# Kernel tuning notes

Hardware: AMD Instinct MI355X
Metric: run time of the kernel (lower is better)

The kernel has to match this reference:

```python
import jax, jax.numpy as jnp
import numpy as np

N = 100000   # nodes
E = 1250000  # directed edges
F = 32       # node_features
H = 64       # hidden_channels
C = 10       # num_classes
NEG_SLOPE = 0.2  # GATConv default LeakyReLU slope


def _glorot(key, shape):
    fan_in = shape[0]
    return jax.random.normal(key, shape, jnp.float32) / np.sqrt(fan_in)


def setup_inputs() -> dict:
    k = jax.random.split(jax.random.key(0), 16)
    x = jax.random.normal(k[0], (N, F), jnp.float32)
    edge_index = jax.random.randint(k[1], (2, E), 0, N, dtype=jnp.int32)
    return {
        "x": x,
        "edge_index": edge_index,
        # GCNConv 1
        "W1": _glorot(k[2], (F, H)), "b1": jnp.zeros((H,), jnp.float32),
        # GATConv (heads=1)
        "W2": _glorot(k[3], (H, H)),
        "a_src": _glorot(k[4], (H,)), "a_dst": _glorot(k[5], (H,)),
        "b2": jnp.zeros((H,), jnp.float32),
        # GCNConv 3
        "W3": _glorot(k[6], (H, H)), "b3": jnp.zeros((H,), jnp.float32),
        # optimization head
        "Wopt": _glorot(k[7], (H, C)), "bopt": jnp.zeros((C,), jnp.float32),
        # bottleneck detector MLP
        "Wb1": _glorot(k[8], (H, 32)), "bb1": jnp.zeros((32,), jnp.float32),
        "Wb2": _glorot(k[9], (32, 1)), "bb2": jnp.zeros((1,), jnp.float32),
    }


def _gcn_conv(x, W, b, src, dst, n):
    # PyG GCNConv: self-loops already appended to src/dst by caller.
    h = x @ W  # [n, out]
    deg = jnp.zeros((n,), x.dtype).at[dst].add(1.0)
    dinv = jax.lax.rsqrt(jnp.maximum(deg, 1e-12))
    norm = dinv[src] * dinv[dst]  # [e]
    msg = h[src] * norm[:, None]  # gather + scale
    out = jnp.zeros_like(h).at[dst].add(msg)  # scatter-add
    return out + b


def _gat_conv(x, W, a_src, a_dst, b, src, dst, n):
    # PyG GATConv, heads=1: self-loops already appended.
    h = x @ W  # [n, out]
    alpha_s = h @ a_src  # [n]
    alpha_d = h @ a_dst  # [n]
    e = jax.nn.leaky_relu(alpha_s[src] + alpha_d[dst], NEG_SLOPE)  # [e]
    # softmax over incoming edges of each dst node
    emax = jax.ops.segment_max(e, dst, num_segments=n)
    p = jnp.exp(e - emax[dst])
    denom = jax.ops.segment_sum(p, dst, num_segments=n)
    alpha = p / denom[dst]
    out = jnp.zeros_like(h).at[dst].add(h[src] * alpha[:, None])
    return out + b


def reference(x, edge_index, W1, b1, W2, a_src, a_dst, b2, W3, b3,
              Wopt, bopt, Wb1, bb1, Wb2, bb2):
    n = x.shape[0]
    loops = jnp.arange(n, dtype=edge_index.dtype)
    src = jnp.concatenate([edge_index[0], loops])
    dst = jnp.concatenate([edge_index[1], loops])

    h = jax.nn.relu(_gcn_conv(x, W1, b1, src, dst, n))
    h = jax.nn.relu(_gat_conv(h, W2, a_src, a_dst, b2, src, dst, n))
    h = jax.nn.relu(_gcn_conv(h, W3, b3, src, dst, n))

    optimizations = h @ Wopt + bopt                     # [n, C]
    bottlenecks = jax.nn.sigmoid(jax.nn.relu(h @ Wb1 + bb1) @ Wb2 + bb2)  # [n, 1]
    graph_embedding = h.mean(axis=0)                    # [H]
    return optimizations, bottlenecks, graph_embedding
```

## Files before the change

### kernel.cpp

```cpp
#include <hip/hip_runtime.h>
#include <hip/hip_bf16.h>


#define CAP 64
#define NP2 128
#define NB2MAX 800

__device__ __forceinline__ int uwave(){
  return __builtin_amdgcn_readfirstlane(threadIdx.x >> 6);
}
__device__ __forceinline__ unsigned short f2bf(float f){
  unsigned u = __float_as_uint(f);
  return (unsigned short)((u + 0x7fffu + ((u >> 16) & 1u)) >> 16);
}
__device__ __forceinline__ float bfl(unsigned u){ return __uint_as_float(u << 16); }
__device__ __forceinline__ float bfh(unsigned u){ return __uint_as_float(u & 0xffff0000u); }
__device__ __forceinline__ float bfu(unsigned short s){ return __uint_as_float(((unsigned)s) << 16); }
__device__ __forceinline__ float rdlane(float v, int l){
  return __uint_as_float(__builtin_amdgcn_readlane(__float_as_uint(v), l));
}

__global__ void k_setup(const float* __restrict__ Wopt, const float* __restrict__ bopt,
                        const float* __restrict__ Wb1, const float* __restrict__ bb1,
                        float* __restrict__ Wcat, float* __restrict__ bcat,
                        int* __restrict__ bcnt, unsigned short* __restrict__ tb,
                        unsigned short* __restrict__ xh, float* __restrict__ emb_acc,
                        float* __restrict__ als, int n, int nb2){
  int i = blockIdx.x*blockDim.x + threadIdx.x;
  if (i < nb2) bcnt[i] = 0;
  if (blockIdx.x == 0){
    int tid = threadIdx.x;
    for (int j = tid; j < 4096; j += 256){
      int f = j >> 6, c = j & 63;
      float w = 0.f;
      if (c < 10)       w = Wopt[f*10 + c];
      else if (c >= 32) w = Wb1[f*32 + (c-32)];
      Wcat[j] = w;
    }
    if (tid < 64){
      float b = 0.f;
      if (tid < 10)       b = bopt[tid];
      else if (tid >= 32) b = bb1[tid-32];
      bcat[tid] = b;
      tb[(size_t)n*64 + tid] = 0;
      emb_acc[tid] = 0.f;
      if (tid == 0) als[n] = 0.f;
    }
    if (tid >= 64 && tid < 96) xh[(size_t)n*32 + (tid-64)] = 0;
  }
}

__global__ __launch_bounds__(256) void k_part(const int* __restrict__ src,
                        const int* __restrict__ dst,
                        uint2* __restrict__ pairs, int* __restrict__ bcnt,
                        int e, int nb2, int pbcap){
  __shared__ int lcnt[NB2MAX];
  __shared__ int lbase[NB2MAX];
  int tid = threadIdx.x;
  for (int j = tid; j < nb2; j += 256) lcnt[j] = 0;
  __syncthreads();
  int i0 = blockIdx.x*2048 + tid*8;
  int d[8], s[8], bk[8], lp[8];
  int nv = e - i0;
  if (nv > 8) nv = 8;
  if (nv < 0) nv = 0;
  if (nv == 8){
    int4 d0 = *(const int4*)(dst + i0), d1 = *(const int4*)(dst + i0 + 4);
    int4 s0 = *(const int4*)(src + i0), s1 = *(const int4*)(src + i0 + 4);
    d[0]=d0.x; d[1]=d0.y; d[2]=d0.z; d[3]=d0.w;
    d[4]=d1.x; d[5]=d1.y; d[6]=d1.z; d[7]=d1.w;
    s[0]=s0.x; s[1]=s0.y; s[2]=s0.z; s[3]=s0.w;
    s[4]=s1.x; s[5]=s1.y; s[6]=s1.z; s[7]=s1.w;
  } else {
    #pragma unroll
    for (int j = 0; j < 8; j++){ d[j] = 0; s[j] = 0; }
    for (int j = 0; j < nv; j++){ d[j] = dst[i0+j]; s[j] = src[i0+j]; }
  }
  #pragma unroll
  for (int j = 0; j < 8; j++){
    if (j < nv){
      bk[j] = d[j] >> 7;
      lp[j] = atomicAdd(&lcnt[bk[j]], 1);
    }
  }
  __syncthreads();
  for (int j = tid; j < nb2; j += 256){
    int c = lcnt[j];
    if (c) lbase[j] = atomicAdd(&bcnt[j], c);
  }
  __syncthreads();
  #pragma unroll
  for (int j = 0; j < 8; j++){
    if (j < nv){
      int p = lbase[bk[j]] + lp[j];
      if (p < pbcap)
        pairs[(size_t)bk[j]*pbcap + p] = make_uint2((unsigned)d[j], (unsigned)s[j]);
    }
  }
}

__global__ __launch_bounds__(256) void k_fill(const uint2* __restrict__ pairs,
                        const int* __restrict__ bcnt, int* __restrict__ cnt,
                        int* __restrict__ adj, int pbcap, int n){
  __shared__ int lc[NP2];
  __shared__ int ladj[NP2*CAP];
  int b = blockIdx.x;
  int lo = b << 7;
  int nn = min(NP2, n - lo);
  int tid = threadIdx.x;
  for (int j = tid; j < NP2; j += 256) lc[j] = 0;
  int4 nfill = make_int4(n, n, n, n);
  for (int j = tid; j < NP2*CAP/4; j += 256) ((int4*)ladj)[j] = nfill;
  __syncthreads();
  int m = bcnt[b];
  if (m > pbcap) m = pbcap;
  const uint2* pb = pairs + (size_t)b*pbcap;
  for (int j = tid; j < m; j += 256){
    uint2 p = pb[j];
    int r = (int)p.x - lo;
    int pos = atomicAdd(&lc[r], 1);
    if (pos < CAP) ladj[(r << 6) + pos] = (int)p.y;
  }
  __syncthreads();
  if (tid < nn) cnt[lo + tid] = lc[tid];
  int tot = nn << 4;
  uint4* ga = (uint4*)(adj + (size_t)lo*CAP);
  const uint4* la = (const uint4*)ladj;
  for (int j = tid; j < tot; j += 256) ga[j] = la[j];
}

__global__ void k_castscale(const float* __restrict__ x, const int* __restrict__ cnt,
                            unsigned short* __restrict__ xh, int total4){
  int i = blockIdx.x*blockDim.x + threadIdx.x;
  if (i >= total4) return;
  int row = i >> 3;
  float dv = rsqrtf((float)(cnt[row] + 1));
  float4 v = ((const float4*)x)[i];
  uint2 o;
  o.x = (unsigned)f2bf(v.x*dv) | ((unsigned)f2bf(v.y*dv) << 16);
  o.y = (unsigned)f2bf(v.z*dv) | ((unsigned)f2bf(v.w*dv) << 16);
  ((uint2*)xh)[i] = o;
}

__global__ __launch_bounds__(256) void k_agg32g(const unsigned short* __restrict__ xh,
                          const int* __restrict__ adj, const int* __restrict__ cnt,
                          const float* __restrict__ W1, const float* __restrict__ b1,
                          unsigned short* __restrict__ h, int n){
  int lane = threadIdx.x & 63;
  float wreg[32];
  #pragma unroll
  for (int k = 0; k < 32; k++) wreg[k] = W1[k*64 + lane];
  float br = b1[lane];
  int v0 = blockIdx.x*8 + uwave()*2;
  if (v0 >= n) return;
  int v1 = v0 + 1;
  bool has1 = v1 < n;
  if (!has1) v1 = v0;
  int cn0 = cnt[v0], cn1 = cnt[v1];
  int c0 = min(cn0, CAP), c1 = min(cn1, CAP);
  int ureg0 = n, ureg1 = n;
  if (lane < c0) ureg0 = (adj + (size_t)v0*CAP)[lane];
  if (lane < c1) ureg1 = (adj + (size_t)v1*CAP)[lane];
  int g = lane >> 3, q = lane & 7;
  float4 a0 = {0.f,0.f,0.f,0.f}, a1 = {0.f,0.f,0.f,0.f};
  int itm = (max(c0, c1) + 7) >> 3;
  #pragma unroll 2
  for (int jj = 0; jj < itm; jj++){
    int u0 = __shfl(ureg0, jj*8 + g);
    int u1 = __shfl(ureg1, jj*8 + g);
    uint2 r0 = ((const uint2*)(xh + (size_t)u0*32))[q];
    uint2 r1 = ((const uint2*)(xh + (size_t)u1*32))[q];
    a0.x += bfl(r0.x); a0.y += bfh(r0.x); a0.z += bfl(r0.y); a0.w += bfh(r0.y);
    a1.x += bfl(r1.x); a1.y += bfh(r1.x); a1.z += bfl(r1.y); a1.w += bfh(r1.y);
  }
  #pragma unroll
  for (int off = 8; off <= 32; off <<= 1){
    a0.x += __shfl_xor(a0.x, off); a0.y += __shfl_xor(a0.y, off);
    a0.z += __shfl_xor(a0.z, off); a0.w += __shfl_xor(a0.w, off);
    a1.x += __shfl_xor(a1.x, off); a1.y += __shfl_xor(a1.y, off);
    a1.z += __shfl_xor(a1.z, off); a1.w += __shfl_xor(a1.w, off);
  }
  uint2 s0 = ((const uint2*)(xh + (size_t)v0*32))[q];
  uint2 s1 = ((const uint2*)(xh + (size_t)v1*32))[q];
  a0.x += bfl(s0.x); a0.y += bfh(s0.x); a0.z += bfl(s0.y); a0.w += bfh(s0.y);
  a1.x += bfl(s1.x); a1.y += bfh(s1.x); a1.z += bfl(s1.y); a1.w += bfh(s1.y);
  float dv0 = rsqrtf((float)(cn0 + 1)), dv1 = rsqrtf((float)(cn1 + 1));
  a0.x *= dv0; a0.y *= dv0; a0.z *= dv0; a0.w *= dv0;
  a1.x *= dv1; a1.y *= dv1; a1.z *= dv1; a1.w *= dv1;
  float h0 = br, h1v = br;
  #pragma unroll
  for (int q2 = 0; q2 < 8; q2++){
    float w0x = rdlane(a0.x, q2), w1x = rdlane(a1.x, q2);
    float w0y = rdlane(a0.y, q2), w1y = rdlane(a1.y, q2);
    float w0z = rdlane(a0.z, q2), w1z = rdlane(a1.z, q2);
    float w0w = rdlane(a0.w, q2), w1w = rdlane(a1.w, q2);
    h0 = fmaf(w0x, wreg[q2*4+0], h0); h1v = fmaf(w1x, wreg[q2*4+0], h1v);
    h0 = fmaf(w0y, wreg[q2*4+1], h0); h1v = fmaf(w1y, wreg[q2*4+1], h1v);
    h0 = fmaf(w0z, wreg[q2*4+2], h0); h1v = fmaf(w1z, wreg[q2*4+2], h1v);
    h0 = fmaf(w0w, wreg[q2*4+3], h0); h1v = fmaf(w1w, wreg[q2*4+3], h1v);
  }
  h[(size_t)v0*64 + lane] = f2bf(fmaxf(h0, 0.f));
  if (has1) h[(size_t)v1*64 + lane] = f2bf(fmaxf(h1v, 0.f));
}

template<bool SCALE>
__global__ __launch_bounds__(256, 4) void k_gemm_b(const unsigned short* __restrict__ x,
                       const float* __restrict__ W, const int* __restrict__ cnt,
                       unsigned short* __restrict__ t, int n){
  int lane = threadIdx.x & 63;
  int gw = blockIdx.x*4 + uwave();
  int nw = gridDim.x*4;
  float wreg[64];
  #pragma unroll
  for (int k = 0; k < 64; k++) wreg[k] = W[k*64 + lane];
  for (int v = gw; v < n; v += nw){
    const uint4* xr = (const uint4*)(x + (size_t)v*64);
    float acc = 0.f;
    #pragma unroll
    for (int k8 = 0; k8 < 8; k8++){
      uint4 c = xr[k8];
      acc = fmaf(bfl(c.x), wreg[k8*8+0], acc);
      acc = fmaf(bfh(c.x), wreg[k8*8+1], acc);
      acc = fmaf(bfl(c.y), wreg[k8*8+2], acc);
      acc = fmaf(bfh(c.y), wreg[k8*8+3], acc);
      acc = fmaf(bfl(c.z), wreg[k8*8+4], acc);
      acc = fmaf(bfh(c.z), wreg[k8*8+5], acc);
      acc = fmaf(bfl(c.w), wreg[k8*8+6], acc);
      acc = fmaf(bfh(c.w), wreg[k8*8+7], acc);
    }
    if (SCALE) acc *= rsqrtf((float)(cnt[v] + 1));
    t[(size_t)v*64 + lane] = f2bf(acc);
  }
}

__global__ __launch_bounds__(256, 4) void k_gemm_alpha(const unsigned short* __restrict__ x,
                       const float* __restrict__ W,
                       const float* __restrict__ asrc, const float* __restrict__ adst,
                       unsigned short* __restrict__ t, float* __restrict__ als,
                       float* __restrict__ ald, int n){
  int lane = threadIdx.x & 63;
  int gw = blockIdx.x*4 + uwave();
  int nw = gridDim.x*4;
  float wreg[64];
  #pragma unroll
  for (int k = 0; k < 64; k++) wreg[k] = W[k*64 + lane];
  float asr = asrc[lane], adr = adst[lane];
  for (int v = gw; v < n; v += nw){
    const uint4* xr = (const uint4*)(x + (size_t)v*64);
    float acc = 0.f;
    #pragma unroll
    for (int k8 = 0; k8 < 8; k8++){
      uint4 c = xr[k8];
      acc = fmaf(bfl(c.x), wreg[k8*8+0], acc);
      acc = fmaf(bfh(c.x), wreg[k8*8+1], acc);
      acc = fmaf(bfl(c.y), wreg[k8*8+2], acc);
      acc = fmaf(bfh(c.y), wreg[k8*8+3], acc);
      acc = fmaf(bfl(c.z), wreg[k8*8+4], acc);
      acc = fmaf(bfh(c.z), wreg[k8*8+5], acc);
      acc = fmaf(bfl(c.w), wreg[k8*8+6], acc);
      acc = fmaf(bfh(c.w), wreg[k8*8+7], acc);
    }
    t[(size_t)v*64 + lane] = f2bf(acc);
    float s1 = acc * asr, s2 = acc * adr;
    #pragma unroll
    for (int off = 32; off; off >>= 1){
      s1 += __shfl_xor(s1, off);
      s2 += __shfl_xor(s2, off);
    }
    if (lane == 0){ als[v] = s1; ald[v] = s2; }
  }
}

__global__ __launch_bounds__(256) void k_gcn_agg(const unsigned short* __restrict__ t,
                          const int* __restrict__ adj, const int* __restrict__ cnt,
                          const float* __restrict__ b, unsigned short* __restrict__ h, int n){
  int lane = threadIdx.x & 63;
  int g = lane >> 3, q = lane & 7;
  int v0 = blockIdx.x*32 + uwave()*8;
  if (v0 >= n) return;
  int vg = v0 + g;
  bool vok = vg < n;
  int vgc = vok ? vg : n - 1;
  int cn = cnt[vgc];
  int c = vok ? min(cn, CAP) : 0;
  int cm = c;
  cm = max(cm, __shfl_xor(cm, 8));
  cm = max(cm, __shfl_xor(cm, 16));
  cm = max(cm, __shfl_xor(cm, 32));
  int cmax = __builtin_amdgcn_readfirstlane(cm);
  const int* arow = adj + (size_t)vgc*CAP;
  float a[8] = {0,0,0,0,0,0,0,0};
  int bsel = (lane & 56);
  for (int blk = 0; blk*8 < cmax; blk++){
    int ureg = arow[blk*8 + q];
    #pragma unroll
    for (int j2 = 0; j2 < 8; j2++){
      if (blk*8 + j2 >= cmax) break;
      int u = __shfl(ureg, bsel | j2);
      uint4 r = ((const uint4*)(t + (size_t)u*64))[q];
      a[0] += bfl(r.x); a[1] += bfh(r.x); a[2] += bfl(r.y); a[3] += bfh(r.y);
      a[4] += bfl(r.z); a[5] += bfh(r.z); a[6] += bfl(r.w); a[7] += bfh(r.w);
    }
  }
  uint4 s = ((const uint4*)(t + (size_t)vgc*64))[q];
  a[0] += bfl(s.x); a[1] += bfh(s.x); a[2] += bfl(s.y); a[3] += bfh(s.y);
  a[4] += bfl(s.z); a[5] += bfh(s.z); a[6] += bfl(s.w); a[7] += bfh(s.w);
  float dv = rsqrtf((float)(cn + 1));
  float4 b0 = ((const float4*)b)[2*q], b1v = ((const float4*)b)[2*q+1];
  float r0 = fmaxf(fmaf(a[0], dv, b0.x), 0.f),  r1 = fmaxf(fmaf(a[1], dv, b0.y), 0.f);
  float r2 = fmaxf(fmaf(a[2], dv, b0.z), 0.f),  r3 = fmaxf(fmaf(a[3], dv, b0.w), 0.f);
  float r4 = fmaxf(fmaf(a[4], dv, b1v.x), 0.f), r5 = fmaxf(fmaf(a[5], dv, b1v.y), 0.f);
  float r6 = fmaxf(fmaf(a[6], dv, b1v.z), 0.f), r7 = fmaxf(fmaf(a[7], dv, b1v.w), 0.f);
  uint4 o;
  o.x = (unsigned)f2bf(r0) | ((unsigned)f2bf(r1) << 16);
  o.y = (unsigned)f2bf(r2) | ((unsigned)f2bf(r3) << 16);
  o.z = (unsigned)f2bf(r4) | ((unsigned)f2bf(r5) << 16);
  o.w = (unsigned)f2bf(r6) | ((unsigned)f2bf(r7) << 16);
  if (vok) ((uint4*)(h + (size_t)vg*64))[q] = o;
}

__global__ __launch_bounds__(256) void k_gat_agg(const unsigned short* __restrict__ t,
                          const int* __restrict__ adj, const int* __restrict__ cnt,
                          const float* __restrict__ als, const float* __restrict__ ald,
                          const float* __restrict__ b, unsigned short* __restrict__ h, int n){
  int lane = threadIdx.x & 63;
  int g = lane >> 3, q = lane & 7;
  int v0 = blockIdx.x*32 + uwave()*8;
  if (v0 >= n) return;
  int vg = v0 + g;
  bool vok = vg < n;
  int vgc = vok ? vg : n - 1;
  int c = vok ? min(cnt[vgc], CAP) : 0;
  int cm = c;
  cm = max(cm, __shfl_xor(cm, 8));
  cm = max(cm, __shfl_xor(cm, 16));
  cm = max(cm, __shfl_xor(cm, 32));
  int cmax = __builtin_amdgcn_readfirstlane(cm);
  const int* arow = adj + (size_t)vgc*CAP;
  float adv = ald[vgc];
  float es = als[vgc] + adv; es = es > 0.f ? es : 0.2f*es;
  float er[8];
  float em = es;
  #pragma unroll
  for (int r = 0; r < 8; r++){
    if (r*8 >= cmax) break;
    int slot = r*8 + q;
    int u = arow[slot];
    float ev = als[u] + adv; ev = ev > 0.f ? ev : 0.2f*ev;
    er[r] = (slot < c) ? ev : -1e30f;
    em = fmaxf(em, er[r]);
  }
  em = fmaxf(em, __shfl_xor(em, 1));
  em = fmaxf(em, __shfl_xor(em, 2));
  em = fmaxf(em, __shfl_xor(em, 4));
  float sm = 0.f;
  #pragma unroll
  for (int r = 0; r < 8; r++){
    if (r*8 >= cmax) break;
    sm += ((r*8 + q) < c) ? __expf(er[r] - em) : 0.f;
  }
  sm += __shfl_xor(sm, 1);
  sm += __shfl_xor(sm, 2);
  sm += __shfl_xor(sm, 4);
  float ps = __expf(es - em);
  float inv = 1.f / (sm + ps);
  float a[8] = {0,0,0,0,0,0,0,0};
  int bsel = (lane & 56);
  for (int blk = 0; blk*8 < cmax; blk++){
    int ureg = arow[blk*8 + q];
    #pragma unroll
    for (int j2 = 0; j2 < 8; j2++){
      if (blk*8 + j2 >= cmax) break;
      int u = __shfl(ureg, bsel | j2);
      float ev = als[u] + adv; ev = ev > 0.f ? ev : 0.2f*ev;
      float w = __expf(ev - em);
      uint4 r = ((const uint4*)(t + (size_t)u*64))[q];
      a[0] = fmaf(w, bfl(r.x), a[0]); a[1] = fmaf(w, bfh(r.x), a[1]);
      a[2] = fmaf(w, bfl(r.y), a[2]); a[3] = fmaf(w, bfh(r.y), a[3]);
      a[4] = fmaf(w, bfl(r.z), a[4]); a[5] = fmaf(w, bfh(r.z), a[5]);
      a[6] = fmaf(w, bfl(r.w), a[6]); a[7] = fmaf(w, bfh(r.w), a[7]);
    }
  }
  uint4 s = ((const uint4*)(t + (size_t)vgc*64))[q];
  a[0] = fmaf(ps, bfl(s.x), a[0]); a[1] = fmaf(ps, bfh(s.x), a[1]);
  a[2] = fmaf(ps, bfl(s.y), a[2]); a[3] = fmaf(ps, bfh(s.y), a[3]);
  a[4] = fmaf(ps, bfl(s.z), a[4]); a[5] = fmaf(ps, bfh(s.z), a[5]);
  a[6] = fmaf(ps, bfl(s.w), a[6]); a[7] = fmaf(ps, bfh(s.w), a[7]);
  float4 b0 = ((const float4*)b)[2*q], b1v = ((const float4*)b)[2*q+1];
  float r0 = fmaxf(fmaf(a[0], inv, b0.x), 0.f),  r1 = fmaxf(fmaf(a[1], inv, b0.y), 0.f);
  float r2 = fmaxf(fmaf(a[2], inv, b0.z), 0.f),  r3 = fmaxf(fmaf(a[3], inv, b0.w), 0.f);
  float r4 = fmaxf(fmaf(a[4], inv, b1v.x), 0.f), r5 = fmaxf(fmaf(a[5], inv, b1v.y), 0.f);
  float r6 = fmaxf(fmaf(a[6], inv, b1v.z), 0.f), r7 = fmaxf(fmaf(a[7], inv, b1v.w), 0.f);
  uint4 o;
  o.x = (unsigned)f2bf(r0) | ((unsigned)f2bf(r1) << 16);
  o.y = (unsigned)f2bf(r2) | ((unsigned)f2bf(r3) << 16);
  o.z = (unsigned)f2bf(r4) | ((unsigned)f2bf(r5) << 16);
  o.w = (unsigned)f2bf(r6) | ((unsigned)f2bf(r7) << 16);
  if (vok) ((uint4*)(h + (size_t)vg*64))[q] = o;
}

__global__ __launch_bounds__(256, 4) void k_heads(const unsigned short* __restrict__ h,
                        const float* __restrict__ Wcat, const float* __restrict__ bcat,
                        const float* __restrict__ Wb2, const float* __restrict__ bb2,
                        float* __restrict__ out_opt, float* __restrict__ out_bot, int n){
  int lane = threadIdx.x & 63;
  int gw = blockIdx.x*4 + uwave();
  int nw = gridDim.x*4;
  float wreg[64];
  #pragma unroll
  for (int k = 0; k < 64; k++) wreg[k] = Wcat[k*64 + lane];
  float bcr  = bcat[lane];
  float wb2r = (lane >= 32) ? Wb2[lane-32] : 0.f;
  float bb2r = bb2[0];
  for (int v = gw; v < n; v += nw){
    const uint4* xr = (const uint4*)(h + (size_t)v*64);
    float acc = bcr;
    #pragma unroll
    for (int k8 = 0; k8 < 8; k8++){
      uint4 c = xr[k8];
      acc = fmaf(bfl(c.x), wreg[k8*8+0], acc);
      acc = fmaf(bfh(c.x), wreg[k8*8+1], acc);
      acc = fmaf(bfl(c.y), wreg[k8*8+2], acc);
      acc = fmaf(bfh(c.y), wreg[k8*8+3], acc);
      acc = fmaf(bfl(c.z), wreg[k8*8+4], acc);
      acc = fmaf(bfh(c.z), wreg[k8*8+5], acc);
      acc = fmaf(bfl(c.w), wreg[k8*8+6], acc);
      acc = fmaf(bfh(c.w), wreg[k8*8+7], acc);
    }
    if (lane < 10) out_opt[(size_t)v*10 + lane] = acc;
    float contrib = fmaxf(acc, 0.f) * wb2r;
    #pragma unroll
    for (int off = 32; off; off >>= 1) contrib += __shfl_xor(contrib, off);
    if (lane == 0) out_bot[v] = 1.f / (1.f + __expf(-(contrib + bb2r)));
  }
}

__global__ __launch_bounds__(256) void k_mean(const unsigned short* __restrict__ h,
                       float* __restrict__ emb_acc, int n){
  __shared__ float red[256];
  int tid = threadIdx.x;
  int w = tid >> 6, lane = tid & 63;
  float s = 0.f;
  for (int r = blockIdx.x*4 + w; r < n; r += 1024)
    s += __uint_as_float(((unsigned)h[(size_t)r*64 + lane]) << 16);
  red[tid] = s;
  __syncthreads();
  if (tid < 64)
    atomicAdd(&emb_acc[tid], red[tid] + red[64+tid] + red[128+tid] + red[192+tid]);
}

__global__ void k_embed(const float* __restrict__ emb_acc, float* __restrict__ out_emb,
                        float invn){
  if (threadIdx.x < 64) out_emb[threadIdx.x] = emb_acc[threadIdx.x] * invn;
}

extern "C" void kernel_launch(void* const* d_in, const int* in_sizes, int n_in,
                              void* d_out, int out_size, void* d_ws, size_t ws_size,
                              hipStream_t stream) {
  const float* x    = (const float*)d_in[0];
  const int*   ei   = (const int*)d_in[1];
  const float* W1   = (const float*)d_in[2];
  const float* b1   = (const float*)d_in[3];
  const float* W2   = (const float*)d_in[4];
  const float* a_s  = (const float*)d_in[5];
  const float* a_d  = (const float*)d_in[6];
  const float* b2   = (const float*)d_in[7];
  const float* W3   = (const float*)d_in[8];
  const float* b3   = (const float*)d_in[9];
  const float* Wopt = (const float*)d_in[10];
  const float* bopt = (const float*)d_in[11];
  const float* Wb1  = (const float*)d_in[12];
  const float* bb1  = (const float*)d_in[13];
  const float* Wb2  = (const float*)d_in[14];
  const float* bb2  = (const float*)d_in[15];

  int n = in_sizes[0] / 32;
  int e = in_sizes[1] / 2;
  const int* src = ei;
  const int* dst = ei + e;

  char* ws = (char*)d_ws;
  size_t off = 0;
  auto alloc = [&](size_t bytes) -> void* {
    void* p = ws + off;
    off += (bytes + 255) & ~(size_t)255;
    return p;
  };
  int nb2 = (n + NP2 - 1) >> 7;
  int*            cnt     = (int*)           alloc((size_t)n * 4);
  int*            adj     = (int*)           alloc((size_t)n * CAP * 4);
  float*          als     = (float*)         alloc((size_t)(n+1) * 4);
  float*          ald     = (float*)         alloc((size_t)n * 4);
  unsigned short* xh      = (unsigned short*)alloc((size_t)(n+1) * 32 * 2);
  unsigned short* tb      = (unsigned short*)alloc((size_t)(n+1) * 64 * 2);
  unsigned short* hbuf    = (unsigned short*)alloc((size_t)n * 64 * 2);
  float*          emb_acc = (float*)         alloc((size_t)64 * 4);
  float*          Wcat    = (float*)         alloc((size_t)4096 * 4);
  float*          bcat    = (float*)         alloc((size_t)64 * 4);
  int*            bcnt    = (int*)           alloc((size_t)nb2 * 4);

  int pbcap = e / nb2 + 384;
  long pcap_max = ((long)n * 128) / ((long)nb2 * 8);
  if (pbcap > (int)pcap_max) pbcap = (int)pcap_max;
  uint2* pairs = (uint2*)hbuf;

  float* out_opt = (float*)d_out;
  float* out_bot = out_opt + (size_t)n * 10;
  float* out_emb = out_bot + n;

  int nb8    = (n + 7) / 8;
  int nbW    = (n + 31) / 32;
  int nbN    = (n + 255) / 256;
  int nbP    = (e + 2047) / 2048;
  int total4 = n*32/4;
  int nbC    = (total4 + 255) / 256;

  k_setup<<<nbN, 256, 0, stream>>>(Wopt, bopt, Wb1, bb1, Wcat, bcat,
                                   bcnt, tb, xh, emb_acc, als, n, nb2);
  k_part<<<nbP, 256, 0, stream>>>(src, dst, pairs, bcnt, e, nb2, pbcap);
  k_fill<<<nb2, 256, 0, stream>>>(pairs, bcnt, cnt, adj, pbcap, n);
  k_castscale<<<nbC, 256, 0, stream>>>(x, cnt, xh, total4);

  k_agg32g<<<nb8, 256, 0, stream>>>(xh, adj, cnt, W1, b1, hbuf, n);

  k_gemm_alpha<<<1024, 256, 0, stream>>>(hbuf, W2, a_s, a_d, tb, als, ald, n);
  k_gat_agg<<<nbW, 256, 0, stream>>>(tb, adj, cnt, als, ald, b2, hbuf, n);

  k_gemm_b<true><<<1024, 256, 0, stream>>>(hbuf, W3, cnt, tb, n);
  k_gcn_agg<<<nbW, 256, 0, stream>>>(tb, adj, cnt, b3, hbuf, n);

  k_heads<<<1024, 256, 0, stream>>>(hbuf, Wcat, bcat, Wb2, bb2,
                                    out_opt, out_bot, n);
  k_mean<<<256, 256, 0, stream>>>(hbuf, emb_acc, n);
  k_embed<<<1, 64, 0, stream>>>(emb_acc, out_emb, 1.0f / (float)n);
}
```

Before: 349.3 us.

## Sort nodes by in-degree to balance wave work and fuse cast into fill

```diff
diff --git a/kernel.cpp b/kernel.cpp
--- a/kernel.cpp
+++ b/kernel.cpp
@@ -15,7 +15,6 @@
 }
 __device__ __forceinline__ float bfl(unsigned u){ return __uint_as_float(u << 16); }
 __device__ __forceinline__ float bfh(unsigned u){ return __uint_as_float(u & 0xffff0000u); }
-__device__ __forceinline__ float bfu(unsigned short s){ return __uint_as_float(((unsigned)s) << 16); }
 __device__ __forceinline__ float rdlane(float v, int l){
   return __uint_as_float(__builtin_amdgcn_readlane(__float_as_uint(v), l));
 }
@@ -23,13 +22,15 @@
 __global__ void k_setup(const float* __restrict__ Wopt, const float* __restrict__ bopt,
                         const float* __restrict__ Wb1, const float* __restrict__ bb1,
                         float* __restrict__ Wcat, float* __restrict__ bcat,
-                        int* __restrict__ bcnt, unsigned short* __restrict__ tb,
+                        int* __restrict__ bcnt, int* __restrict__ ghist,
+                        unsigned short* __restrict__ tb,
                         unsigned short* __restrict__ xh, float* __restrict__ emb_acc,
                         float* __restrict__ als, int n, int nb2){
   int i = blockIdx.x*blockDim.x + threadIdx.x;
   if (i < nb2) bcnt[i] = 0;
+  int tid = threadIdx.x;
+  if (blockIdx.x == 1 && tid < 65) ghist[tid] = 0;
   if (blockIdx.x == 0){
-    int tid = threadIdx.x;
     for (int j = tid; j < 4096; j += 256){
       int f = j >> 6, c = j & 63;
       float w = 0.f;
@@ -101,14 +102,18 @@
 
 __global__ __launch_bounds__(256) void k_fill(const uint2* __restrict__ pairs,
                         const int* __restrict__ bcnt, int* __restrict__ cnt,
-                        int* __restrict__ adj, int pbcap, int n){
+                        int* __restrict__ adj, int* __restrict__ ghist,
+                        const float* __restrict__ x, unsigned short* __restrict__ xh,
+                        int pbcap, int n){
   __shared__ int lc[NP2];
   __shared__ int ladj[NP2*CAP];
+  __shared__ int lh[65];
   int b = blockIdx.x;
   int lo = b << 7;
   int nn = min(NP2, n - lo);
   int tid = threadIdx.x;
   for (int j = tid; j < NP2; j += 256) lc[j] = 0;
+  if (tid < 65) lh[tid] = 0;
   int4 nfill = make_int4(n, n, n, n);
   for (int j = tid; j < NP2*CAP/4; j += 256) ((int4*)ladj)[j] = nfill;
   __syncthreads();
@@ -122,28 +127,58 @@
     if (pos < CAP) ladj[(r << 6) + pos] = (int)p.y;
   }
   __syncthreads();
-  if (tid < nn) cnt[lo + tid] = lc[tid];
+  if (tid < nn){
+    int c = lc[tid];
+    cnt[lo + tid] = c;
+    atomicAdd(&lh[min(c, CAP)], 1);
+  }
+  __syncthreads();
+  if (tid < 65 && lh[tid]) atomicAdd(&ghist[tid], lh[tid]);
   int tot = nn << 4;
   uint4* ga = (uint4*)(adj + (size_t)lo*CAP);
   const uint4* la = (const uint4*)ladj;
   for (int j = tid; j < tot; j += 256) ga[j] = la[j];
-}
-
-__global__ void k_castscale(const float* __restrict__ x, const int* __restrict__ cnt,
-                            unsigned short* __restrict__ xh, int total4){
-  int i = blockIdx.x*blockDim.x + threadIdx.x;
-  if (i >= total4) return;
-  int row = i >> 3;
-  float dv = rsqrtf((float)(cnt[row] + 1));
-  float4 v = ((const float4*)x)[i];
-  uint2 o;
-  o.x = (unsigned)f2bf(v.x*dv) | ((unsigned)f2bf(v.y*dv) << 16);
-  o.y = (unsigned)f2bf(v.z*dv) | ((unsigned)f2bf(v.w*dv) << 16);
-  ((uint2*)xh)[i] = o;
+  int tf = nn << 3;
+  const float4* xr4 = (const float4*)(x + (size_t)lo*32);
+  uint2* xo = (uint2*)(xh + (size_t)lo*32);
+  for (int j = tid; j < tf; j += 256){
+    int r = j >> 3;
+    float dv = rsqrtf((float)(lc[r] + 1));
+    float4 v = xr4[j];
+    uint2 o;
+    o.x = (unsigned)f2bf(v.x*dv) | ((unsigned)f2bf(v.y*dv) << 16);
+    o.y = (unsigned)f2bf(v.z*dv) | ((unsigned)f2bf(v.w*dv) << 16);
+    xo[j] = o;
+  }
+}
+
+__global__ void k_scan(const int* __restrict__ ghist, int* __restrict__ dbase){
+  if (threadIdx.x == 0){
+    int s = 0;
+    for (int d = 0; d < 65; d++){ dbase[d] = s; s += ghist[d]; }
+  }
+}
+
+__global__ __launch_bounds__(256) void k_perm(const int* __restrict__ cnt,
+                        int* __restrict__ dbase, int* __restrict__ perm, int n){
+  __shared__ int lh[65];
+  __shared__ int lb[65];
+  int tid = threadIdx.x;
+  int v = blockIdx.x*256 + tid;
+  if (tid < 65) lh[tid] = 0;
+  __syncthreads();
+  int d = 0, lp = 0;
+  bool ok = v < n;
+  if (ok){ d = min(cnt[v], CAP); lp = atomicAdd(&lh[d], 1); }
+  __syncthreads();
+  if (tid < 65 && lh[tid]) lb[tid] = atomicAdd(&dbase[tid], lh[tid]);
+  __syncthreads();
+  if (ok) perm[lb[d] + lp] = v;
 }
 
 __global__ __launch_bounds__(256) void k_agg32g(const unsigned short* __restrict__ xh,
                           const int* __restrict__ adj, const int* __restrict__ cnt,
+                          const int* __restrict__ perm,
                           const float* __restrict__ W1, const float* __restrict__ b1,
                           unsigned short* __restrict__ h, int n){
   int lane = threadIdx.x & 63;
@@ -151,11 +186,12 @@
   #pragma unroll
   for (int k = 0; k < 32; k++) wreg[k] = W1[k*64 + lane];
   float br = b1[lane];
-  int v0 = blockIdx.x*8 + uwave()*2;
-  if (v0 >= n) return;
-  int v1 = v0 + 1;
-  bool has1 = v1 < n;
-  if (!has1) v1 = v0;
+  int i0 = blockIdx.x*8 + uwave()*2;
+  if (i0 >= n) return;
+  int i1 = i0 + 1;
+  bool has1 = i1 < n;
+  int v0 = perm[i0];
+  int v1 = perm[has1 ? i1 : i0];
   int cn0 = cnt[v0], cn1 = cnt[v1];
   int c0 = min(cn0, CAP), c1 = min(cn1, CAP);
   int ureg0 = n, ureg1 = n;
@@ -273,22 +309,23 @@
 
 __global__ __launch_bounds__(256) void k_gcn_agg(const unsigned short* __restrict__ t,
                           const int* __restrict__ adj, const int* __restrict__ cnt,
+                          const int* __restrict__ perm,
                           const float* __restrict__ b, unsigned short* __restrict__ h, int n){
   int lane = threadIdx.x & 63;
   int g = lane >> 3, q = lane & 7;
-  int v0 = blockIdx.x*32 + uwave()*8;
-  if (v0 >= n) return;
-  int vg = v0 + g;
-  bool vok = vg < n;
-  int vgc = vok ? vg : n - 1;
-  int cn = cnt[vgc];
+  int i0 = blockIdx.x*32 + uwave()*8;
+  if (i0 >= n) return;
+  int idx = i0 + g;
+  bool vok = idx < n;
+  int vg = perm[vok ? idx : n - 1];
+  int cn = cnt[vg];
   int c = vok ? min(cn, CAP) : 0;
   int cm = c;
   cm = max(cm, __shfl_xor(cm, 8));
   cm = max(cm, __shfl_xor(cm, 16));
   cm = max(cm, __shfl_xor(cm, 32));
   int cmax = __builtin_amdgcn_readfirstlane(cm);
-  const int* arow = adj + (size_t)vgc*CAP;
+  const int* arow = adj + (size_t)vg*CAP;
   float a[8] = {0,0,0,0,0,0,0,0};
   int bsel = (lane & 56);
   for (int blk = 0; blk*8 < cmax; blk++){
@@ -302,7 +339,7 @@
       a[4] += bfl(r.z); a[5] += bfh(r.z); a[6] += bfl(r.w); a[7] += bfh(r.w);
     }
   }
-  uint4 s = ((const uint4*)(t + (size_t)vgc*64))[q];
+  uint4 s = ((const uint4*)(t + (size_t)vg*64))[q];
   a[0] += bfl(s.x); a[1] += bfh(s.x); a[2] += bfl(s.y); a[3] += bfh(s.y);
   a[4] += bfl(s.z); a[5] += bfh(s.z); a[6] += bfl(s.w); a[7] += bfh(s.w);
   float dv = rsqrtf((float)(cn + 1));
@@ -321,24 +358,25 @@
 
 __global__ __launch_bounds__(256) void k_gat_agg(const unsigned short* __restrict__ t,
                           const int* __restrict__ adj, const int* __restrict__ cnt,
+                          const int* __restrict__ perm,
                           const float* __restrict__ als, const float* __restrict__ ald,
                           const float* __restrict__ b, unsigned short* __restrict__ h, int n){
   int lane = threadIdx.x & 63;
   int g = lane >> 3, q = lane & 7;
-  int v0 = blockIdx.x*32 + uwave()*8;
-  if (v0 >= n) return;
-  int vg = v0 + g;
-  bool vok = vg < n;
-  int vgc = vok ? vg : n - 1;
-  int c = vok ? min(cnt[vgc], CAP) : 0;
+  int i0 = blockIdx.x*32 + uwave()*8;
+  if (i0 >= n) return;
+  int idx = i0 + g;
+  bool vok = idx < n;
+  int vg = perm[vok ? idx : n - 1];
+  int c = vok ? min(cnt[vg], CAP) : 0;
   int cm = c;
   cm = max(cm, __shfl_xor(cm, 8));
   cm = max(cm, __shfl_xor(cm, 16));
   cm = max(cm, __shfl_xor(cm, 32));
   int cmax = __builtin_amdgcn_readfirstlane(cm);
-  const int* arow = adj + (size_t)vgc*CAP;
-  float adv = ald[vgc];
-  float es = als[vgc] + adv; es = es > 0.f ? es : 0.2f*es;
+  const int* arow = adj + (size_t)vg*CAP;
+  float adv = ald[vg];
+  float es = als[vg] + adv; es = es > 0.f ? es : 0.2f*es;
   float er[8];
   float em = es;
   #pragma unroll
@@ -381,7 +419,7 @@
       a[6] = fmaf(w, bfl(r.w), a[6]); a[7] = fmaf(w, bfh(r.w), a[7]);
     }
   }
-  uint4 s = ((const uint4*)(t + (size_t)vgc*64))[q];
+  uint4 s = ((const uint4*)(t + (size_t)vg*64))[q];
   a[0] = fmaf(ps, bfl(s.x), a[0]); a[1] = fmaf(ps, bfh(s.x), a[1]);
   a[2] = fmaf(ps, bfl(s.y), a[2]); a[3] = fmaf(ps, bfh(s.y), a[3]);
   a[4] = fmaf(ps, bfl(s.z), a[4]); a[5] = fmaf(ps, bfh(s.z), a[5]);
@@ -498,6 +536,9 @@
   float*          Wcat    = (float*)         alloc((size_t)4096 * 4);
   float*          bcat    = (float*)         alloc((size_t)64 * 4);
   int*            bcnt    = (int*)           alloc((size_t)nb2 * 4);
+  int*            ghist   = (int*)           alloc((size_t)65 * 4);
+  int*            dbase   = (int*)           alloc((size_t)65 * 4);
+  int*            perm    = (int*)           alloc((size_t)n * 4);
 
   int pbcap = e / nb2 + 384;
   long pcap_max = ((long)n * 128) / ((long)nb2 * 8);
@@ -512,22 +553,21 @@
   int nbW    = (n + 31) / 32;
   int nbN    = (n + 255) / 256;
   int nbP    = (e + 2047) / 2048;
-  int total4 = n*32/4;
-  int nbC    = (total4 + 255) / 256;
 
   k_setup<<<nbN, 256, 0, stream>>>(Wopt, bopt, Wb1, bb1, Wcat, bcat,
-                                   bcnt, tb, xh, emb_acc, als, n, nb2);
+                                   bcnt, ghist, tb, xh, emb_acc, als, n, nb2);
   k_part<<<nbP, 256, 0, stream>>>(src, dst, pairs, bcnt, e, nb2, pbcap);
-  k_fill<<<nb2, 256, 0, stream>>>(pairs, bcnt, cnt, adj, pbcap, n);
-  k_castscale<<<nbC, 256, 0, stream>>>(x, cnt, xh, total4);
-
-  k_agg32g<<<nb8, 256, 0, stream>>>(xh, adj, cnt, W1, b1, hbuf, n);
+  k_fill<<<nb2, 256, 0, stream>>>(pairs, bcnt, cnt, adj, ghist, x, xh, pbcap, n);
+  k_scan<<<1, 64, 0, stream>>>(ghist, dbase);
+  k_perm<<<nbN, 256, 0, stream>>>(cnt, dbase, perm, n);
+
+  k_agg32g<<<nb8, 256, 0, stream>>>(xh, adj, cnt, perm, W1, b1, hbuf, n);
 
   k_gemm_alpha<<<1024, 256, 0, stream>>>(hbuf, W2, a_s, a_d, tb, als, ald, n);
-  k_gat_agg<<<nbW, 256, 0, stream>>>(tb, adj, cnt, als, ald, b2, hbuf, n);
+  k_gat_agg<<<nbW, 256, 0, stream>>>(tb, adj, cnt, perm, als, ald, b2, hbuf, n);
 
   k_gemm_b<true><<<1024, 256, 0, stream>>>(hbuf, W3, cnt, tb, n);
-  k_gcn_agg<<<nbW, 256, 0, stream>>>(tb, adj, cnt, b3, hbuf, n);
+  k_gcn_agg<<<nbW, 256, 0, stream>>>(tb, adj, cnt, perm, b3, hbuf, n);
 
   k_heads<<<1024, 256, 0, stream>>>(hbuf, Wcat, bcat, Wb2, bb2,
                                     out_opt, out_bot, n);
```

Result: slower. 357.6 us (+2.4%).
